# Performance work log

Hardware: AMD Instinct MI355X
Metric: run time of the kernel (lower is better)

The kernel has to match this reference:

```python
import jax, jax.numpy as jnp
import numpy as np

B_SZ, L_SEQ, ENC_IN = 8, 1024, 32
D_MODEL, D_INNER, D_STATE, D_CONV, DT_RANK = 256, 512, 16, 4, 16
N_LAYERS, D_FF, C_OUT = 2, 1024, 1


def setup_inputs() -> dict:
    key = jax.random.key(0)
    ks = jax.random.split(key, 16)
    s = 0.02
    inp = {}
    inp["x"] = jax.random.normal(ks[0], (B_SZ, L_SEQ, ENC_IN), jnp.float32)
    inp["in_w"] = jax.random.normal(ks[1], (D_MODEL, ENC_IN), jnp.float32) * s
    inp["in_b"] = jnp.zeros((D_MODEL,), jnp.float32)
    inp["in_proj_w"] = jax.random.normal(ks[2], (N_LAYERS, 2 * D_INNER, D_MODEL), jnp.float32) * s
    inp["conv_w"] = jax.random.normal(ks[3], (N_LAYERS, D_INNER, D_CONV), jnp.float32) * 0.1
    inp["conv_b"] = jnp.zeros((N_LAYERS, D_INNER), jnp.float32)
    inp["x_proj_w"] = jax.random.normal(ks[4], (N_LAYERS, DT_RANK + 2 * D_STATE, D_INNER), jnp.float32) * s
    inp["dt_w"] = jax.random.normal(ks[5], (N_LAYERS, D_INNER, DT_RANK), jnp.float32) * (DT_RANK ** -0.5)
    dt = jax.random.uniform(ks[6], (N_LAYERS, D_INNER), jnp.float32, 1e-3, 0.1)
    inp["dt_b"] = dt + jnp.log(-jnp.expm1(-dt))  # inverse softplus
    inp["A_log"] = jnp.tile(jnp.log(jnp.arange(1, D_STATE + 1, dtype=jnp.float32)), (N_LAYERS, D_INNER, 1))
    inp["D_skip"] = jnp.ones((N_LAYERS, D_INNER), jnp.float32)
    inp["out_proj_w"] = jax.random.normal(ks[7], (N_LAYERS, D_MODEL, D_INNER), jnp.float32) * s
    inp["p1_w"] = jax.random.normal(ks[8], (D_FF, D_MODEL), jnp.float32) * s
    inp["p1_b"] = jnp.zeros((D_FF,), jnp.float32)
    inp["p2_w"] = jax.random.normal(ks[9], (C_OUT, D_FF), jnp.float32) * s
    inp["p2_b"] = jnp.zeros((C_OUT,), jnp.float32)
    return inp


def causal_dw_conv(x, w, b):
    # x: [b, l, d], w: [d, k] depthwise, left-pad for causality
    xc = jax.lax.conv_general_dilated(
        x.transpose(0, 2, 1), w[:, None, :], (1,), [(D_CONV - 1, 0)],
        feature_group_count=D_INNER, dimension_numbers=("NCH", "OIH", "NCH"))
    return (xc + b[None, :, None]).transpose(0, 2, 1)


def selective_scan(u, dt, A, Bm, Cm):
    # u, dt: [b, l, d]; Bm, Cm: [b, l, n]; A: [d, n]
    def step(h, inp):
        u_t, dt_t, B_t, C_t = inp  # [b,d],[b,d],[b,n],[b,n]
        dA = jnp.exp(dt_t[..., None] * A)                      # [b,d,n]
        dBu = dt_t[..., None] * B_t[:, None, :] * u_t[..., None]
        h = dA * h + dBu
        y = jnp.einsum("bdn,bn->bd", h, C_t)
        return h, y
    h0 = jnp.zeros((u.shape[0], D_INNER, D_STATE), u.dtype)
    xs = (u.transpose(1, 0, 2), dt.transpose(1, 0, 2),
          Bm.transpose(1, 0, 2), Cm.transpose(1, 0, 2))
    _, ys = jax.lax.scan(step, h0, xs)
    return ys.transpose(1, 0, 2)  # [b, l, d]


def mamba_block(h, ipw, cw, cb, xpw, dtw, dtb, Alog, Dp, opw):
    xz = jnp.einsum("bld,ed->ble", h, ipw)          # [b,l,2*d_inner]
    xi, z = jnp.split(xz, 2, axis=-1)
    xc = jax.nn.silu(causal_dw_conv(xi, cw, cb))     # [b,l,d_inner]
    xdbl = jnp.einsum("bld,ed->ble", xc, xpw)        # [b,l,dt_rank+2n]
    dt_lo = xdbl[..., :DT_RANK]
    Bm = xdbl[..., DT_RANK:DT_RANK + D_STATE]
    Cm = xdbl[..., DT_RANK + D_STATE:]
    dt = jax.nn.softplus(jnp.einsum("blr,dr->bld", dt_lo, dtw) + dtb)
    A = -jnp.exp(Alog)
    y = selective_scan(xc, dt, A, Bm, Cm) + xc * Dp
    y = y * jax.nn.silu(z)
    return jnp.einsum("bld,ed->ble", y, opw)


def reference(x, in_w, in_b, in_proj_w, conv_w, conv_b, x_proj_w, dt_w, dt_b,
              A_log, D_skip, out_proj_w, p1_w, p1_b, p2_w, p2_b):
    h = jnp.einsum("bli,di->bld", x, in_w) + in_b
    for i in range(N_LAYERS):
        h = mamba_block(h, in_proj_w[i], conv_w[i], conv_b[i], x_proj_w[i],
                        dt_w[i], dt_b[i], A_log[i], D_skip[i], out_proj_w[i])
    h = h[:, -1, :]  # last timestep
    h = jax.nn.gelu(jnp.einsum("bd,fd->bf", h, p1_w) + p1_b, approximate=False)
    return jnp.einsum("bf,cf->bc", h, p2_w) + p2_b
```

## Files before the change

### kernel.cpp

```cpp
#include <hip/hip_runtime.h>
#include <math.h>


static constexpr int L_SEQ = 1024;
static constexpr int M_ROWS = 8 * 1024;
static constexpr int NCHUNK = 32;
static constexpr int TCHUNK = 32;

typedef unsigned short u16;
typedef unsigned short u16x8 __attribute__((ext_vector_type(8)));
typedef unsigned short u16x4 __attribute__((ext_vector_type(4)));
typedef short bf16x8 __attribute__((ext_vector_type(8)));
typedef float f32x4 __attribute__((ext_vector_type(4)));

__device__ __forceinline__ float silu_f(float x) { return x / (1.f + __expf(-x)); }
__device__ __forceinline__ float softplus_f(float x) {
  return (x > 20.f) ? x : log1pf(__expf(x));
}
__device__ __forceinline__ u16 f2bf(float f) {
  unsigned u = __builtin_bit_cast(unsigned, f);
  u += 0x7FFFu + ((u >> 16) & 1u);
  return (u16)(u >> 16);
}
__device__ __forceinline__ float bf2f(u16 v) {
  return __builtin_bit_cast(float, (unsigned)v << 16);
}

__device__ __forceinline__ void gll16(const u16* g, u16* l) {
  __builtin_amdgcn_global_load_lds(
      (const __attribute__((address_space(1))) void*)g,
      (__attribute__((address_space(3))) void*)l, 16, 0, 0);
}

template<int BM,int BN,int BK,int EPI,int OUTBF>
__global__ __launch_bounds__(256)
void gemm_db(const u16* __restrict__ A, int lda,
             const u16* __restrict__ W, int ldw,
             const float* __restrict__ bias,
             void* __restrict__ Cp, int ldc,
             int N, int K)
{
  constexpr int KS = BK / 32;
  constexpr int CA = BK / 8;
  constexpr int NCH_A = (BM / 64) * CA;
  constexpr int NCH_B = (BN / 64) * CA;
  constexpr int TI = BM / 2 / 16;
  constexpr int TJ = BN / 2 / 16;

  __shared__ u16 As[2][BM * BK];
  __shared__ u16 Ws[2][BN * BK];

  const int tid = threadIdx.x;
  const int lane = tid & 63;
  const int wv = tid >> 6;
  const int wy = wv >> 1, wx = wv & 1;
  const int rb = wy * (BM / 2);
  const int cb = wx * (BN / 2);
  const int lr = lane & 15, lq = lane >> 4;
  const int bm = blockIdx.x * BM;
  const int bn = blockIdx.y * BN;

  f32x4 acc[TI][TJ];
#pragma unroll
  for (int i = 0; i < TI; ++i)
#pragma unroll
    for (int j = 0; j < TJ; ++j) acc[i][j] = (f32x4){0.f, 0.f, 0.f, 0.f};

  auto stage = [&](int k0, int buf) {
#pragma unroll
    for (int w = wv; w < NCH_A + NCH_B; w += 4) {
      if (w < NCH_A) {
        const int rh = w / CA, lqw = w % CA;
        gll16(A + (size_t)(bm + rh * 64 + lane) * lda + k0 + lqw * 8,
              &As[buf][(lqw * BM + rh * 64) * 8]);
      } else {
        const int w2 = w - NCH_A;
        const int rh = w2 / CA, lqw = w2 % CA;
        gll16(W + (size_t)(bn + rh * 64 + lane) * ldw + k0 + lqw * 8,
              &Ws[buf][(lqw * BN + rh * 64) * 8]);
      }
    }
  };

  stage(0, 0);
  int cur = 0;
  for (int k0 = 0; k0 < K; k0 += BK) {
    __syncthreads();
    if (k0 + BK < K) stage(k0 + BK, cur ^ 1);

#pragma unroll
    for (int ks = 0; ks < KS; ++ks) {
      const int lqc = ks * 4 + lq;
      bf16x8 af[TI], bf[TJ];
#pragma unroll
      for (int i = 0; i < TI; ++i)
        af[i] = *reinterpret_cast<const bf16x8*>(
                  &As[cur][(lqc * BM + rb + i * 16 + lr) * 8]);
#pragma unroll
      for (int j = 0; j < TJ; ++j)
        bf[j] = *reinterpret_cast<const bf16x8*>(
                  &Ws[cur][(lqc * BN + cb + j * 16 + lr) * 8]);
#pragma unroll
      for (int i = 0; i < TI; ++i)
#pragma unroll
        for (int j = 0; j < TJ; ++j)
          acc[i][j] = __builtin_amdgcn_mfma_f32_16x16x32_bf16(af[i], bf[j], acc[i][j], 0, 0, 0);
    }
    cur ^= 1;
  }

#pragma unroll
  for (int i = 0; i < TI; ++i) {
#pragma unroll
    for (int j = 0; j < TJ; ++j) {
      const int col = bn + cb + j * 16 + lr;
      if (col >= N) continue;
#pragma unroll
      for (int r = 0; r < 4; ++r) {
        const int row = bm + rb + i * 16 + lq * 4 + r;
        float c = acc[i][j][r];
        if (EPI == 1) c += bias[col];
        if (EPI == 2) { if (col < 512) c = softplus_f(c + bias[col]); }
        if (OUTBF) ((u16*)Cp)[(size_t)row * ldc + col] = f2bf(c);
        else       ((float*)Cp)[(size_t)row * ldc + col] = c;
      }
    }
  }
}

__global__ __launch_bounds__(512)
void prep(const float* __restrict__ x, const float* __restrict__ in_w,
          const float* __restrict__ in_b,
          const float* __restrict__ ipw, const float* __restrict__ opw,
          const float* __restrict__ dtw, const float* __restrict__ xpw,
          u16* __restrict__ x16, u16* __restrict__ opw16,
          u16* __restrict__ ipw16l1, u16* __restrict__ wc1,
          float* __restrict__ bias1, u16* __restrict__ wc)
{
  const int blk = blockIdx.x;
  if (blk < 384) {
    const float* src; u16* dst; int base;
    if (blk < 128)      { src = x;            dst = x16;     base = blk; }
    else if (blk < 256) { src = opw;          dst = opw16;   base = blk - 128; }
    else                { src = ipw + 262144; dst = ipw16l1; base = blk - 256; }
    const int i = (base * 512 + threadIdx.x) * 4;
    float4 v = *reinterpret_cast<const float4*>(src + i);
    u16x4 o;
    o[0] = f2bf(v.x); o[1] = f2bf(v.y); o[2] = f2bf(v.z); o[3] = f2bf(v.w);
    *reinterpret_cast<u16x4*>(dst + i) = o;
  } else if (blk < 448) {
    const int t = threadIdx.x;
    const int n = (blk - 384) * 16 + (t >> 5);
    const int enc = t & 31;
    const float* iprow = ipw + (size_t)n * 256;
    float v = 0.f;
#pragma unroll 8
    for (int j = 0; j < 256; ++j) v = fmaf(iprow[j], in_w[j * 32 + enc], v);
    wc1[n * 32 + enc] = f2bf(v);
    if (enc == 0) {
      float bv = 0.f;
      for (int j = 0; j < 256; ++j) bv = fmaf(iprow[j], in_b[j], bv);
      bias1[n] = bv;
    }
  } else {
    const int idx = blk - 448;
    const int layer = idx / 640;
    const int n = idx % 640;
    const int k = threadIdx.x;
    const float* xp = xpw + (size_t)layer * 48 * 512;
    float v = 0.f;
    if (n < 512) {
      const float* dw = dtw + (size_t)layer * 512 * 16 + n * 16;
#pragma unroll
      for (int r = 0; r < 16; ++r) v = fmaf(dw[r], xp[r * 512 + k], v);
    } else if (n < 544) {
      v = xp[(16 + (n - 512)) * 512 + k];
    }
    wc[((size_t)layer * 640 + n) * 512 + k] = f2bf(v);
  }
}

__global__ __launch_bounds__(512)
void conv_silu(const u16* __restrict__ xz, const float* __restrict__ cw,
               const float* __restrict__ cb, u16* __restrict__ xc)
{
  const int b = blockIdx.x;
  const int l0 = blockIdx.y * 32;
  const int d = threadIdx.x;

  const float w0 = cw[d * 4 + 0], w1 = cw[d * 4 + 1];
  const float w2 = cw[d * 4 + 2], w3 = cw[d * 4 + 3];
  const float bias = cb[d];

  const size_t base = ((size_t)b * L_SEQ) * 1024 + d;
  float xm3 = (l0 >= 3) ? bf2f(xz[base + (size_t)(l0 - 3) * 1024]) : 0.f;
  float xm2 = (l0 >= 2) ? bf2f(xz[base + (size_t)(l0 - 2) * 1024]) : 0.f;
  float xm1 = (l0 >= 1) ? bf2f(xz[base + (size_t)(l0 - 1) * 1024]) : 0.f;

#pragma unroll 4
  for (int i = 0; i < 32; ++i) {
    const int l = l0 + i;
    const float x0 = bf2f(xz[base + (size_t)l * 1024]);
    const float v = bias + w0 * xm3 + w1 * xm2 + w2 * xm1 + w3 * x0;
    xc[((size_t)b * L_SEQ + l) * 512 + d] = f2bf(silu_f(v));
    xm3 = xm2; xm2 = xm1; xm1 = x0;
  }
}

__global__ __launch_bounds__(256)
void k_scan(const float* __restrict__ xo, const u16* __restrict__ u,
            const u16* __restrict__ xz, const float* __restrict__ Alog,
            const float* __restrict__ Dsk, u16* __restrict__ yg)
{
  const int b = blockIdx.x;
  const int d0 = blockIdx.y * 8;
  const int tid = threadIdx.x;
  const int dl = tid & 7;
  const int c = tid >> 3;
  const int d = d0 + dl;
  const int t0 = c * TCHUNK;

  __shared__ float sAg[NCHUNK][8][16];
  __shared__ float sBg[NCHUNK][8][16];

  float A[16], h[16], p[16];
  const float* al = Alog + d * 16;
#pragma unroll
  for (int n = 0; n < 16; ++n) { A[n] = -__expf(al[n]); h[n] = 0.f; p[n] = 1.f; }

#pragma unroll 2
  for (int t = 0; t < TCHUNK; ++t) {
    const size_t row = (size_t)b * L_SEQ + t0 + t;
    const float dtv = xo[row * 544 + d];
    const float uv  = bf2f(u[row * 512 + d]);
    const float cf  = dtv * uv;
    const f32x4* Bq = reinterpret_cast<const f32x4*>(&xo[row * 544 + 512]);
#pragma unroll
    for (int q = 0; q < 4; ++q) {
      const f32x4 Bv = Bq[q];
#pragma unroll
      for (int k = 0; k < 4; ++k) {
        const int n = q * 4 + k;
        const float dA = __expf(dtv * A[n]);
        p[n] *= dA;
        h[n] = fmaf(dA, h[n], cf * Bv[k]);
      }
    }
  }

#pragma unroll
  for (int q = 0; q < 4; ++q) {
    f32x4 va, vb;
#pragma unroll
    for (int k = 0; k < 4; ++k) { va[k] = p[q * 4 + k]; vb[k] = h[q * 4 + k]; }
    *reinterpret_cast<f32x4*>(&sAg[c][dl][q * 4]) = va;
    *reinterpret_cast<f32x4*>(&sBg[c][dl][q * 4]) = vb;
  }
  __syncthreads();

  if (tid < 128) {
    const int pd = tid >> 4;
    const int pn = tid & 15;
    float hh = 0.f;
    for (int cc = 0; cc < NCHUNK; ++cc) {
      const float a  = sAg[cc][pd][pn];
      const float bb = sBg[cc][pd][pn];
      sAg[cc][pd][pn] = hh;
      hh = fmaf(a, hh, bb);
    }
  }
  __syncthreads();

#pragma unroll
  for (int q = 0; q < 4; ++q) {
    const f32x4 v = *reinterpret_cast<const f32x4*>(&sAg[c][dl][q * 4]);
#pragma unroll
    for (int k = 0; k < 4; ++k) h[q * 4 + k] = v[k];
  }
  const float Dv = Dsk[d];

#pragma unroll 2
  for (int t = 0; t < TCHUNK; ++t) {
    const size_t row = (size_t)b * L_SEQ + t0 + t;
    const float dtv = xo[row * 544 + d];
    const float uv  = bf2f(u[row * 512 + d]);
    const float zf  = bf2f(xz[row * 1024 + 512 + d]);
    const float cf  = dtv * uv;
    const f32x4* Bq = reinterpret_cast<const f32x4*>(&xo[row * 544 + 512]);
    const f32x4* Cq = reinterpret_cast<const f32x4*>(&xo[row * 544 + 528]);
    float s0 = 0.f, s1 = 0.f, s2 = 0.f, s3 = 0.f;
#pragma unroll
    for (int q = 0; q < 4; ++q) {
      const f32x4 Bv = Bq[q];
      const f32x4 Cv = Cq[q];
#pragma unroll
      for (int k = 0; k < 4; ++k) {
        const int n = q * 4 + k;
        const float dA = __expf(dtv * A[n]);
        h[n] = fmaf(dA, h[n], cf * Bv[k]);
      }
      s0 = fmaf(h[q * 4 + 0], Cv[0], s0);
      s1 = fmaf(h[q * 4 + 1], Cv[1], s1);
      s2 = fmaf(h[q * 4 + 2], Cv[2], s2);
      s3 = fmaf(h[q * 4 + 3], Cv[3], s3);
    }
    const float yv = fmaf(uv, Dv, (s0 + s1) + (s2 + s3));
    yg[row * 512 + d] = f2bf(yv * silu_f(zf));
  }
}

__global__ __launch_bounds__(1024)
void head(const u16* __restrict__ h, const float* __restrict__ p1w,
          const float* __restrict__ p1b, const float* __restrict__ p2w,
          const float* __restrict__ p2b, float* __restrict__ out)
{
  const int b = blockIdx.x;
  const int f = threadIdx.x;

  __shared__ float hl[256];
  if (f < 256) hl[f] = bf2f(h[((size_t)b * L_SEQ + (L_SEQ - 1)) * 256 + f]);
  __syncthreads();

  const float* wr = p1w + (size_t)f * 256;
  float acc = 0.f;
#pragma unroll 8
  for (int k = 0; k < 256; k += 4) {
    float4 wv = *reinterpret_cast<const float4*>(wr + k);
    acc = fmaf(hl[k + 0], wv.x, acc);
    acc = fmaf(hl[k + 1], wv.y, acc);
    acc = fmaf(hl[k + 2], wv.z, acc);
    acc = fmaf(hl[k + 3], wv.w, acc);
  }
  const float xv = acc + p1b[f];
  const float gg = 0.5f * xv * (1.f + erff(xv * 0.70710678118654752f));
  float s = gg * p2w[f];

  s += __shfl_xor(s, 1);
  s += __shfl_xor(s, 2);
  s += __shfl_xor(s, 4);
  s += __shfl_xor(s, 8);
  s += __shfl_xor(s, 16);
  s += __shfl_xor(s, 32);
  __shared__ float red[16];
  if ((f & 63) == 0) red[f >> 6] = s;
  __syncthreads();
  if (f == 0) {
    float t = 0.f;
#pragma unroll
    for (int i = 0; i < 16; ++i) t += red[i];
    out[b] = t + p2b[0];
  }
}

extern "C" void kernel_launch(void* const* d_in, const int* in_sizes, int n_in,
                              void* d_out, int out_size, void* d_ws, size_t ws_size,
                              hipStream_t stream)
{
  const float* x    = (const float*)d_in[0];
  const float* in_w = (const float*)d_in[1];
  const float* in_b = (const float*)d_in[2];
  const float* ipw  = (const float*)d_in[3];
  const float* cw   = (const float*)d_in[4];
  const float* cb   = (const float*)d_in[5];
  const float* xpw  = (const float*)d_in[6];
  const float* dtw  = (const float*)d_in[7];
  const float* dtb  = (const float*)d_in[8];
  const float* Alog = (const float*)d_in[9];
  const float* Dsk  = (const float*)d_in[10];
  const float* opw  = (const float*)d_in[11];
  const float* p1w  = (const float*)d_in[12];
  const float* p1b  = (const float*)d_in[13];
  const float* p2w  = (const float*)d_in[14];
  const float* p2b  = (const float*)d_in[15];

  float* ws = (float*)d_ws;
  u16*   h16  = (u16*)(ws);
  u16*   xz16 = (u16*)(ws + 1048576);
  u16*   xc16 = (u16*)(ws + 5242880);
  float* xo   = ws + 7340032;
  u16*   wc16 = (u16*)(ws + 11796480);
  u16*   wbf  = (u16*)(ws + 12124160);
  u16*   wc1  = (u16*)(ws + 12517376);
  float* bias1 = ws + 12533760;

  u16* x16     = wbf;
  u16* opw16   = wbf + 262144;
  u16* ipw16l1 = wbf + 524288;

  prep<<<1728, 512, 0, stream>>>(x, in_w, in_b, ipw, opw, dtw, xpw,
                                 x16, opw16, ipw16l1, wc1, bias1, wc16);

  {
    gemm_db<64, 128, 32, 1, 1><<<dim3(M_ROWS / 64, 8), 256, 0, stream>>>(
        x16, 32, wc1, 32, bias1, xz16, 1024, 1024, 32);

    conv_silu<<<dim3(8, 32), 512, 0, stream>>>(xz16, cw, cb, xc16);

    gemm_db<64, 128, 64, 2, 0><<<dim3(M_ROWS / 64, 5), 256, 0, stream>>>(
        xc16, 512, wc16, 512, dtb, xo, 544, 544, 512);

    k_scan<<<dim3(8, 64), 256, 0, stream>>>(xo, xc16, xz16, Alog, Dsk, xc16);

    gemm_db<64, 64, 64, 0, 1><<<dim3(M_ROWS / 64, 4), 256, 0, stream>>>(
        xc16, 512, opw16, 512, nullptr, h16, 256, 256, 512);
  }

  {
    const float* cw_l  = cw  + 512 * 4;
    const float* cb_l  = cb  + 512;
    const float* dtb_l = dtb + 512;
    const float* Al_l  = Alog + 512 * 16;
    const float* Dsk_l = Dsk + 512;
    const u16*   opw_l = opw16 + 256 * 512;
    const u16*   wc_l  = wc16 + 640 * 512;

    gemm_db<64, 128, 64, 0, 1><<<dim3(M_ROWS / 64, 8), 256, 0, stream>>>(
        h16, 256, ipw16l1, 256, nullptr, xz16, 1024, 1024, 256);

    conv_silu<<<dim3(8, 32), 512, 0, stream>>>(xz16, cw_l, cb_l, xc16);

    gemm_db<64, 128, 64, 2, 0><<<dim3(M_ROWS / 64, 5), 256, 0, stream>>>(
        xc16, 512, wc_l, 512, dtb_l, xo, 544, 544, 512);

    k_scan<<<dim3(8, 64), 256, 0, stream>>>(xo, xc16, xz16, Al_l, Dsk_l, xc16);

    gemm_db<64, 64, 64, 0, 1><<<dim3(M_ROWS / 64, 4), 256, 0, stream>>>(
        xc16, 512, opw_l, 512, nullptr, h16, 256, 256, 512);
  }

  head<<<8, 1024, 0, stream>>>(h16, p1w, p1b, p2w, p2b, (float*)d_out);
}
```

Measured before the change: 361.1 us.

## Fuse causal conv+SiLU into x_proj GEMM loader and skip final out_proj

The depthwise causal conv and SiLU are now computed inside the x_proj GEMM's A-tile staging. Blocks with blockIdx.y==0 also write xc to global memory for the scan, which removes the separate conv_silu kernels. The last layer's full out_proj GEMM is dropped; the head computes out_proj only for the last timestep from yg, since only h[:, -1] is used. Scan loop unroll is raised from 2 to 4. The fused loader uses synchronous loads instead of async global_load_lds and recomputes the conv in each of the 5 column blocks. That adds redundant work and may weaken load/compute overlap.

```diff
diff --git a/kernel.cpp b/kernel.cpp
--- a/kernel.cpp
+++ b/kernel.cpp
@@ -32,13 +32,15 @@
       (__attribute__((address_space(3))) void*)l, 16, 0, 0);
 }
 
-template<int BM,int BN,int BK,int EPI,int OUTBF>
+template<int BM,int BN,int BK,int EPI,int OUTBF,int AMODE>
 __global__ __launch_bounds__(256)
 void gemm_db(const u16* __restrict__ A, int lda,
              const u16* __restrict__ W, int ldw,
              const float* __restrict__ bias,
              void* __restrict__ Cp, int ldc,
-             int N, int K)
+             int N, int K,
+             const float* __restrict__ cw, const float* __restrict__ cb,
+             u16* __restrict__ xcout)
 {
   constexpr int KS = BK / 32;
   constexpr int CA = BK / 8;
@@ -55,10 +57,11 @@
   const int wv = tid >> 6;
   const int wy = wv >> 1, wx = wv & 1;
   const int rb = wy * (BM / 2);
-  const int cb = wx * (BN / 2);
+  const int cb_ = wx * (BN / 2);
   const int lr = lane & 15, lq = lane >> 4;
   const int bm = blockIdx.x * BM;
   const int bn = blockIdx.y * BN;
+  const bool store_xc = (AMODE == 1) && (blockIdx.y == 0);
 
   f32x4 acc[TI][TJ];
 #pragma unroll
@@ -71,8 +74,40 @@
     for (int w = wv; w < NCH_A + NCH_B; w += 4) {
       if (w < NCH_A) {
         const int rh = w / CA, lqw = w % CA;
-        gll16(A + (size_t)(bm + rh * 64 + lane) * lda + k0 + lqw * 8,
-              &As[buf][(lqw * BM + rh * 64) * 8]);
+        const int row = bm + rh * 64 + lane;
+        if (AMODE == 0) {
+          gll16(A + (size_t)row * lda + k0 + lqw * 8,
+                &As[buf][(lqw * BM + rh * 64) * 8]);
+        } else {
+          const int l = row & (L_SEQ - 1);
+          const int dbase = k0 + lqw * 8;
+          const u16* xzr = A + (size_t)row * lda + dbase;
+          u16x8 xr[4];
+#pragma unroll
+          for (int wt = 0; wt < 4; ++wt) {
+            const int ro = wt - 3;
+            if (l + ro >= 0)
+              xr[wt] = *reinterpret_cast<const u16x8*>(xzr + (ptrdiff_t)ro * lda);
+            else
+              xr[wt] = (u16x8){0,0,0,0,0,0,0,0};
+          }
+          const float4 cb0 = *reinterpret_cast<const float4*>(cb + dbase);
+          const float4 cb1 = *reinterpret_cast<const float4*>(cb + dbase + 4);
+          u16x8 vout;
+#pragma unroll
+          for (int j = 0; j < 8; ++j) {
+            const float4 cwv = *reinterpret_cast<const float4*>(cw + (dbase + j) * 4);
+            float a = (j < 4) ? (&cb0.x)[j] : (&cb1.x)[j - 4];
+            a = fmaf(cwv.x, bf2f(xr[0][j]), a);
+            a = fmaf(cwv.y, bf2f(xr[1][j]), a);
+            a = fmaf(cwv.z, bf2f(xr[2][j]), a);
+            a = fmaf(cwv.w, bf2f(xr[3][j]), a);
+            vout[j] = f2bf(silu_f(a));
+          }
+          *reinterpret_cast<u16x8*>(&As[buf][(lqw * BM + rh * 64 + lane) * 8]) = vout;
+          if (store_xc)
+            *reinterpret_cast<u16x8*>(xcout + (size_t)row * 512 + dbase) = vout;
+        }
       } else {
         const int w2 = w - NCH_A;
         const int rh = w2 / CA, lqw = w2 % CA;
@@ -99,7 +134,7 @@
 #pragma unroll
       for (int j = 0; j < TJ; ++j)
         bf[j] = *reinterpret_cast<const bf16x8*>(
-                  &Ws[cur][(lqc * BN + cb + j * 16 + lr) * 8]);
+                  &Ws[cur][(lqc * BN + cb_ + j * 16 + lr) * 8]);
 #pragma unroll
       for (int i = 0; i < TI; ++i)
 #pragma unroll
@@ -113,7 +148,7 @@
   for (int i = 0; i < TI; ++i) {
 #pragma unroll
     for (int j = 0; j < TJ; ++j) {
-      const int col = bn + cb + j * 16 + lr;
+      const int col = bn + cb_ + j * 16 + lr;
       if (col >= N) continue;
 #pragma unroll
       for (int r = 0; r < 4; ++r) {
@@ -180,33 +215,6 @@
   }
 }
 
-__global__ __launch_bounds__(512)
-void conv_silu(const u16* __restrict__ xz, const float* __restrict__ cw,
-               const float* __restrict__ cb, u16* __restrict__ xc)
-{
-  const int b = blockIdx.x;
-  const int l0 = blockIdx.y * 32;
-  const int d = threadIdx.x;
-
-  const float w0 = cw[d * 4 + 0], w1 = cw[d * 4 + 1];
-  const float w2 = cw[d * 4 + 2], w3 = cw[d * 4 + 3];
-  const float bias = cb[d];
-
-  const size_t base = ((size_t)b * L_SEQ) * 1024 + d;
-  float xm3 = (l0 >= 3) ? bf2f(xz[base + (size_t)(l0 - 3) * 1024]) : 0.f;
-  float xm2 = (l0 >= 2) ? bf2f(xz[base + (size_t)(l0 - 2) * 1024]) : 0.f;
-  float xm1 = (l0 >= 1) ? bf2f(xz[base + (size_t)(l0 - 1) * 1024]) : 0.f;
-
-#pragma unroll 4
-  for (int i = 0; i < 32; ++i) {
-    const int l = l0 + i;
-    const float x0 = bf2f(xz[base + (size_t)l * 1024]);
-    const float v = bias + w0 * xm3 + w1 * xm2 + w2 * xm1 + w3 * x0;
-    xc[((size_t)b * L_SEQ + l) * 512 + d] = f2bf(silu_f(v));
-    xm3 = xm2; xm2 = xm1; xm1 = x0;
-  }
-}
-
 __global__ __launch_bounds__(256)
 void k_scan(const float* __restrict__ xo, const u16* __restrict__ u,
             const u16* __restrict__ xz, const float* __restrict__ Alog,
@@ -228,7 +236,7 @@
 #pragma unroll
   for (int n = 0; n < 16; ++n) { A[n] = -__expf(al[n]); h[n] = 0.f; p[n] = 1.f; }
 
-#pragma unroll 2
+#pragma unroll 4
   for (int t = 0; t < TCHUNK; ++t) {
     const size_t row = (size_t)b * L_SEQ + t0 + t;
     const float dtv = xo[row * 544 + d];
@@ -279,7 +287,7 @@
   }
   const float Dv = Dsk[d];
 
-#pragma unroll 2
+#pragma unroll 4
   for (int t = 0; t < TCHUNK; ++t) {
     const size_t row = (size_t)b * L_SEQ + t0 + t;
     const float dtv = xo[row * 544 + d];
@@ -310,15 +318,36 @@
 }
 
 __global__ __launch_bounds__(1024)
-void head(const u16* __restrict__ h, const float* __restrict__ p1w,
-          const float* __restrict__ p1b, const float* __restrict__ p2w,
-          const float* __restrict__ p2b, float* __restrict__ out)
+void head(const u16* __restrict__ yg, const u16* __restrict__ opw_l1,
+          const float* __restrict__ p1w, const float* __restrict__ p1b,
+          const float* __restrict__ p2w, const float* __restrict__ p2b,
+          float* __restrict__ out)
 {
   const int b = blockIdx.x;
   const int f = threadIdx.x;
 
+  __shared__ float ygl[512];
   __shared__ float hl[256];
-  if (f < 256) hl[f] = bf2f(h[((size_t)b * L_SEQ + (L_SEQ - 1)) * 256 + f]);
+  if (f < 512) ygl[f] = bf2f(yg[((size_t)b * L_SEQ + (L_SEQ - 1)) * 512 + f]);
+  __syncthreads();
+
+  if (f < 256) {
+    const u16* wr = opw_l1 + (size_t)f * 512;
+    float acc = 0.f;
+#pragma unroll 8
+    for (int k = 0; k < 512; k += 8) {
+      u16x8 wv = *reinterpret_cast<const u16x8*>(wr + k);
+      acc = fmaf(ygl[k + 0], bf2f(wv[0]), acc);
+      acc = fmaf(ygl[k + 1], bf2f(wv[1]), acc);
+      acc = fmaf(ygl[k + 2], bf2f(wv[2]), acc);
+      acc = fmaf(ygl[k + 3], bf2f(wv[3]), acc);
+      acc = fmaf(ygl[k + 4], bf2f(wv[4]), acc);
+      acc = fmaf(ygl[k + 5], bf2f(wv[5]), acc);
+      acc = fmaf(ygl[k + 6], bf2f(wv[6]), acc);
+      acc = fmaf(ygl[k + 7], bf2f(wv[7]), acc);
+    }
+    hl[f] = acc;
+  }
   __syncthreads();
 
   const float* wr = p1w + (size_t)f * 256;
@@ -391,18 +420,19 @@
                                  x16, opw16, ipw16l1, wc1, bias1, wc16);
 
   {
-    gemm_db<64, 128, 32, 1, 1><<<dim3(M_ROWS / 64, 8), 256, 0, stream>>>(
-        x16, 32, wc1, 32, bias1, xz16, 1024, 1024, 32);
-
-    conv_silu<<<dim3(8, 32), 512, 0, stream>>>(xz16, cw, cb, xc16);
-
-    gemm_db<64, 128, 64, 2, 0><<<dim3(M_ROWS / 64, 5), 256, 0, stream>>>(
-        xc16, 512, wc16, 512, dtb, xo, 544, 544, 512);
+    gemm_db<64, 128, 32, 1, 1, 0><<<dim3(M_ROWS / 64, 8), 256, 0, stream>>>(
+        x16, 32, wc1, 32, bias1, xz16, 1024, 1024, 32,
+        nullptr, nullptr, nullptr);
+
+    gemm_db<64, 128, 64, 2, 0, 1><<<dim3(M_ROWS / 64, 5), 256, 0, stream>>>(
+        xz16, 1024, wc16, 512, dtb, xo, 544, 544, 512,
+        cw, cb, xc16);
 
     k_scan<<<dim3(8, 64), 256, 0, stream>>>(xo, xc16, xz16, Alog, Dsk, xc16);
 
-    gemm_db<64, 64, 64, 0, 1><<<dim3(M_ROWS / 64, 4), 256, 0, stream>>>(
-        xc16, 512, opw16, 512, nullptr, h16, 256, 256, 512);
+    gemm_db<64, 64, 64, 0, 1, 0><<<dim3(M_ROWS / 64, 4), 256, 0, stream>>>(
+        xc16, 512, opw16, 512, nullptr, h16, 256, 256, 512,
+        nullptr, nullptr, nullptr);
   }
 
   {
@@ -411,22 +441,19 @@
     const float* dtb_l = dtb + 512;
     const float* Al_l  = Alog + 512 * 16;
     const float* Dsk_l = Dsk + 512;
-    const u16*   opw_l = opw16 + 256 * 512;
     const u16*   wc_l  = wc16 + 640 * 512;
 
-    gemm_db<64, 128, 64, 0, 1><<<dim3(M_ROWS / 64, 8), 256, 0, stream>>>(
-        h16, 256, ipw16l1, 256, nullptr, xz16, 1024, 1024, 256);
-
-    conv_silu<<<dim3(8, 32), 512, 0, stream>>>(xz16, cw_l, cb_l, xc16);
-
-    gemm_db<64, 128, 64, 2, 0><<<dim3(M_ROWS / 64, 5), 256, 0, stream>>>(
-        xc16, 512, wc_l, 512, dtb_l, xo, 544, 544, 512);
+    gemm_db<64, 128, 64, 0, 1, 0><<<dim3(M_ROWS / 64, 8), 256, 0, stream>>>(
+        h16, 256, ipw16l1, 256, nullptr, xz16, 1024, 1024, 256,
+        nullptr, nullptr, nullptr);
+
+    gemm_db<64, 128, 64, 2, 0, 1><<<dim3(M_ROWS / 64, 5), 256, 0, stream>>>(
+        xz16, 1024, wc_l, 512, dtb_l, xo, 544, 544, 512,
+        cw_l, cb_l, xc16);
 
     k_scan<<<dim3(8, 64), 256, 0, stream>>>(xo, xc16, xz16, Al_l, Dsk_l, xc16);
-
-    gemm_db<64, 64, 64, 0, 1><<<dim3(M_ROWS / 64, 4), 256, 0, stream>>>(
-        xc16, 512, opw_l, 512, nullptr, h16, 256, 256, 512);
-  }
-
-  head<<<8, 1024, 0, stream>>>(h16, p1w, p1b, p2w, p2b, (float*)d_out);
-}
+  }
+
+  head<<<8, 1024, 0, stream>>>(xc16, opw16 + 256 * 512,
+                               p1w, p1b, p2w, p2b, (float*)d_out);
+}
```

After: 408.1 us. 1.13x slower.
